# Kernel optimization log

Measured on AMD Instinct MI355X. Metric: run time of the kernel, lower is better.

## Reference

```python
import jax, jax.numpy as jnp
import numpy as np

B, N, H = 4, 1024, 64

def setup_inputs() -> dict:
    key = jax.random.key(0)
    k1, k2, k3 = jax.random.split(key, 3)
    x = jax.random.normal(k1, (B, N, H), dtype=jnp.float32)
    # nn.Linear(2H, H): weight [H, 2H], bias [H]
    s1 = 1.0 / np.sqrt(2 * H)
    W1 = jax.random.uniform(k2, (H, 2 * H), minval=-s1, maxval=s1, dtype=jnp.float32)
    b1 = jnp.zeros((H,), dtype=jnp.float32)
    # nn.Linear(H, 1): weight [1, H], bias [1]
    s2 = 1.0 / np.sqrt(H)
    W2 = jax.random.uniform(k3, (1, H), minval=-s2, maxval=s2, dtype=jnp.float32)
    b2 = jnp.zeros((1,), dtype=jnp.float32)
    return {"x": x, "W1": W1, "b1": b1, "W2": W2, "b2": b2}

def reference(x, W1, b1, W2, b2):
    # cat([x_i, x_j]) @ W1.T == x_i @ W1a.T + x_j @ W1b.T  (decomposed; same math)
    W1a, W1b = W1[:, :x.shape[-1]], W1[:, x.shape[-1]:]
    hi = jnp.einsum('bid,hd->bih', x, W1a)            # [B,N,H]
    hj = jnp.einsum('bjd,hd->bjh', x, W1b)            # [B,N,H]
    h = jax.nn.relu(hi[:, :, None, :] + hj[:, None, :, :] + b1)  # [B,N,N,H]
    logits = jnp.einsum('bijh,h->bij', h, W2[0]) + b2[0]          # [B,N,N]
    attn = jax.nn.softmax(logits, axis=-1)
    updated = jnp.einsum('bij,bjd->bid', attn, x)     # [B,N,H]
    return updated, attn
```

## Files before the change

### kernel.cpp

```cpp
#include <hip/hip_runtime.h>

#define ATTN_OFF 262144

#define WS_HIP  0
#define WS_HJP  131072

typedef float4 f4;
typedef _Float16 h2v __attribute__((ext_vector_type(2)));

union F4H { f4 f; h2v h[4]; };
union F2H { float2 f; h2v h[2]; };

__device__ __forceinline__ f4 ld4(const float* p) { return *reinterpret_cast<const f4*>(p); }
__device__ __forceinline__ void st4(float* p, f4 v) { *reinterpret_cast<f4*>(p) = v; }
__device__ __forceinline__ float fdot2f(h2v a, h2v b, float c) {
    return __builtin_amdgcn_fdot2(a, b, c, false);
}
__device__ __forceinline__ h2v pack2(float a, float b) {
    h2v r; r.x = (_Float16)a; r.y = (_Float16)b; return r;
}

__global__ __launch_bounds__(256, 4)
void ka_proj(const float* __restrict__ x, const float* __restrict__ W1,
             const float* __restrict__ b1,
             h2v* __restrict__ hiP, h2v* __restrict__ hjP) {
    __shared__ float xT[64 * 36];
    __shared__ float w1T[64 * 68];
    const int t  = threadIdx.x;
    const int i0 = blockIdx.x * 32;
    const int b  = blockIdx.y;
    const int z  = blockIdx.z;
    const int lo = t & 15;
    const int dq = t >> 4;
#pragma unroll
    for (int p = 0; p < 2; ++p) {
        const int il = p * 16 + lo;
        f4 v = ld4(&x[(size_t)(b * 1024 + i0 + il) * 64 + dq * 4]);
        xT[(dq * 4 + 0) * 36 + il] = v.x;
        xT[(dq * 4 + 1) * 36 + il] = v.y;
        xT[(dq * 4 + 2) * 36 + il] = v.z;
        xT[(dq * 4 + 3) * 36 + il] = v.w;
    }
#pragma unroll
    for (int p = 0; p < 4; ++p) {
        const int cl = p * 16 + lo;
        f4 w = ld4(&W1[(size_t)cl * 128 + z * 64 + dq * 4]);
        w1T[(dq * 4 + 0) * 68 + cl] = w.x;
        w1T[(dq * 4 + 1) * 68 + cl] = w.y;
        w1T[(dq * 4 + 2) * 68 + cl] = w.z;
        w1T[(dq * 4 + 3) * 68 + cl] = w.w;
    }
    __syncthreads();
    const int tx = t & 15;
    const int ty = t >> 4;
    float acc[2][4];
    if (z == 0) {
        f4 bv = ld4(&b1[tx * 4]);
        acc[0][0] = acc[1][0] = bv.x;
        acc[0][1] = acc[1][1] = bv.y;
        acc[0][2] = acc[1][2] = bv.z;
        acc[0][3] = acc[1][3] = bv.w;
    } else {
#pragma unroll
        for (int ii = 0; ii < 2; ++ii)
#pragma unroll
            for (int cc = 0; cc < 4; ++cc) acc[ii][cc] = 0.f;
    }
#pragma unroll 8
    for (int d = 0; d < 64; ++d) {
        const float2 xv = *reinterpret_cast<const float2*>(&xT[d * 36 + ty * 2]);
        const f4 wv = ld4(&w1T[d * 68 + tx * 4]);
        acc[0][0] = fmaf(xv.x, wv.x, acc[0][0]);
        acc[0][1] = fmaf(xv.x, wv.y, acc[0][1]);
        acc[0][2] = fmaf(xv.x, wv.z, acc[0][2]);
        acc[0][3] = fmaf(xv.x, wv.w, acc[0][3]);
        acc[1][0] = fmaf(xv.y, wv.x, acc[1][0]);
        acc[1][1] = fmaf(xv.y, wv.y, acc[1][1]);
        acc[1][2] = fmaf(xv.y, wv.z, acc[1][2]);
        acc[1][3] = fmaf(xv.y, wv.w, acc[1][3]);
    }
    h2v* outp = z ? hjP : hiP;
#pragma unroll
    for (int p = 0; p < 2; ++p) {
        F2H uo;
        uo.h[0] = pack2(acc[0][p * 2], acc[0][p * 2 + 1]);
        uo.h[1] = pack2(acc[1][p * 2], acc[1][p * 2 + 1]);
        *reinterpret_cast<float2*>(
            &outp[(size_t)(b * 32 + tx * 2 + p) * 1024 + i0 + ty * 2]) = uo.f;
    }
}

__global__ __launch_bounds__(256, 2)
void kf_fused(const h2v* __restrict__ hiP, const h2v* __restrict__ hjP,
              const float* __restrict__ W2, const float* __restrict__ x,
              float* __restrict__ attn, float* __restrict__ upd) {
    __shared__ union __align__(16) U {
        h2v   hj[32 * 256];
        h2v   xc[128 * 68];
        float red[16 * 516];
    } u;
    __shared__ __align__(16) h2v s_p[512 * 12];
    __shared__ h2v s_hi[32 * 8];
    __shared__ h2v s_w2[32];
    __shared__ float s_il[8];

    const int t  = threadIdx.x;
    const int i0 = blockIdx.x * 8;
    const int b  = blockIdx.y;
    const int w  = t >> 6;
    const int ln = t & 63;
    {
        const int hp = t >> 3, r = t & 7;
        s_hi[hp * 8 + r] = hiP[(size_t)(b * 32 + hp) * 1024 + i0 + r];
    }
    if (t < 16) {
        f4 wq = ld4(&W2[t * 4]);
        s_w2[t * 2]     = pack2(wq.x, wq.y);
        s_w2[t * 2 + 1] = pack2(wq.z, wq.w);
    }
    float l[2][4][4];
#pragma unroll
    for (int r = 0; r < 2; ++r)
#pragma unroll
        for (int c = 0; c < 4; ++c)
#pragma unroll
            for (int k = 0; k < 4; ++k) l[r][c][k] = 0.f;
    h2v hiR[2][32], w2R[32];
    const h2v z2 = (h2v)0;
#pragma unroll
    for (int c = 0; c < 4; ++c) {
#pragma unroll
        for (int p = 0; p < 8; ++p) {
            const int s = p * 256 + t;
            const int hp = s >> 6, j4 = (s & 63) * 4;
            st4((float*)&u.hj[hp * 256 + j4],
                ld4((const float*)&hjP[(size_t)(b * 32 + hp) * 1024 + c * 256 + j4]));
        }
        __syncthreads();
        if (c == 0) {
#pragma unroll
            for (int hp = 0; hp < 32; ++hp) {
                hiR[0][hp] = s_hi[hp * 8 + w];
                hiR[1][hp] = s_hi[hp * 8 + w + 4];
                w2R[hp]    = s_w2[hp];
            }
        }
#pragma unroll
        for (int hp = 0; hp < 32; ++hp) {
            F4H bb;
            bb.f = ld4((const float*)&u.hj[hp * 256 + ln * 4]);
            const h2v wv = w2R[hp];
#pragma unroll
            for (int r = 0; r < 2; ++r) {
                const h2v hv = hiR[r][hp];
#pragma unroll
                for (int k = 0; k < 4; ++k) {
                    h2v rr = __builtin_elementwise_max(hv + bb.h[k], z2);
                    l[r][c][k] = fdot2f(rr, wv, l[r][c][k]);
                }
            }
        }
        __syncthreads();
    }
    float il[2];
#pragma unroll
    for (int r = 0; r < 2; ++r) {
        float m = l[r][0][0];
#pragma unroll
        for (int c = 0; c < 4; ++c)
#pragma unroll
            for (int k = 0; k < 4; ++k) m = fmaxf(m, l[r][c][k]);
#pragma unroll
        for (int d = 1; d < 64; d <<= 1) m = fmaxf(m, __shfl_xor(m, d));
        float sum = 0.f;
#pragma unroll
        for (int c = 0; c < 4; ++c)
#pragma unroll
            for (int k = 0; k < 4; ++k) {
                l[r][c][k] = __expf(l[r][c][k] - m);
                sum += l[r][c][k];
            }
#pragma unroll
        for (int d = 1; d < 64; d <<= 1) sum += __shfl_xor(sum, d);
        il[r] = 1.0f / sum;
    }
    if (ln == 0) { s_il[w] = il[0]; s_il[w + 4] = il[1]; }
#pragma unroll
    for (int r = 0; r < 2; ++r) {
        const int row = w + r * 4;
        const size_t arow = (size_t)(b * 1024 + i0 + row) * 1024 + ln * 4;
#pragma unroll
        for (int c = 0; c < 4; ++c) {
            st4(&attn[arow + c * 256],
                make_float4(l[r][c][0] * il[r], l[r][c][1] * il[r],
                            l[r][c][2] * il[r], l[r][c][3] * il[r]));
            const int jp = c * 128 + ln * 2;
            s_p[jp * 12 + row]       = pack2(l[r][c][0], l[r][c][1]);
            s_p[(jp + 1) * 12 + row] = pack2(l[r][c][2], l[r][c][3]);
        }
    }
    const int dq = t & 15, js = t >> 4;
    float acc[8][4];
#pragma unroll
    for (int i = 0; i < 8; ++i)
#pragma unroll
        for (int q = 0; q < 4; ++q) acc[i][q] = 0.f;
#pragma unroll
    for (int c2 = 0; c2 < 4; ++c2) {
        __syncthreads();
#pragma unroll
        for (int p = 0; p < 8; ++p) {
            const int s = p * 256 + t;
            const int jpl = s >> 4, dd = (s & 15) * 4;
            const float* xr = &x[(size_t)(b * 1024 + c2 * 256 + jpl * 2) * 64 + dd];
            f4 r0 = ld4(xr);
            f4 r1 = ld4(xr + 64);
            F4H pk;
            pk.h[0] = pack2(r0.x, r1.x); pk.h[1] = pack2(r0.y, r1.y);
            pk.h[2] = pack2(r0.z, r1.z); pk.h[3] = pack2(r0.w, r1.w);
            st4((float*)&u.xc[jpl * 68 + dd], pk.f);
        }
        __syncthreads();
#pragma unroll 2
        for (int u8 = 0; u8 < 8; ++u8) {
            const int jpl = u8 * 16 + js;
            const int jp  = c2 * 128 + jpl;
            F4H p0, p1, xv;
            p0.f = ld4((const float*)&s_p[jp * 12]);
            p1.f = ld4((const float*)&s_p[jp * 12 + 4]);
            xv.f = ld4((const float*)&u.xc[jpl * 68 + dq * 4]);
#pragma unroll
            for (int i = 0; i < 8; ++i) {
                const h2v pa = (i < 4) ? p0.h[i] : p1.h[i - 4];
#pragma unroll
                for (int q = 0; q < 4; ++q)
                    acc[i][q] = fdot2f(pa, xv.h[q], acc[i][q]);
            }
        }
    }
    __syncthreads();
#pragma unroll
    for (int i = 0; i < 8; ++i)
        st4(&u.red[js * 516 + i * 64 + dq * 4],
            make_float4(acc[i][0], acc[i][1], acc[i][2], acc[i][3]));
    __syncthreads();
    if (t < 128) {
        const int i = t >> 4, dqq = t & 15;
        f4 a = ld4(&u.red[i * 64 + dqq * 4]);
#pragma unroll
        for (int js2 = 1; js2 < 16; ++js2) {
            f4 v = ld4(&u.red[js2 * 516 + i * 64 + dqq * 4]);
            a.x += v.x; a.y += v.y; a.z += v.z; a.w += v.w;
        }
        const float sc = s_il[i];
        st4(&upd[(size_t)(b * 1024 + i0 + i) * 64 + dqq * 4],
            make_float4(a.x * sc, a.y * sc, a.z * sc, a.w * sc));
    }
}

extern "C" void kernel_launch(void* const* d_in, const int* in_sizes, int n_in,
                              void* d_out, int out_size, void* d_ws, size_t ws_size,
                              hipStream_t stream) {
    const float* x  = (const float*)d_in[0];
    const float* W1 = (const float*)d_in[1];
    const float* b1 = (const float*)d_in[2];
    const float* W2 = (const float*)d_in[3];
    float* out = (float*)d_out;
    float* ws  = (float*)d_ws;
    h2v* hiP = (h2v*)(ws + WS_HIP);
    h2v* hjP = (h2v*)(ws + WS_HJP);

    ka_proj <<<dim3(32, 4, 2), 256, 0, stream>>>(x, W1, b1, hiP, hjP);
    kf_fused<<<dim3(128, 4),   256, 0, stream>>>(hiP, hjP, W2, x, out + ATTN_OFF, out);
}
```

Measured before the change: 99.16 us.

## Prefetch hj tiles in registers, read x directly, and shrink shared memory

The projection kernel now writes hi in row-major transposed form and pre-packs W2 to fp16 in the workspace, so the fused kernel loads hi and W2 straight into registers instead of going through shared memory. The hj tile loop register-prefetches the next chunk while the current one is computed, removing one load/store sync per chunk. The attn·x phase drops the shared-memory x staging and reads and packs x from global memory per wave. The cross-thread reduction moves to shuffles plus a small shared buffer. Shared-memory use falls, which may raise occupancy, but the change adds register pressure and repeated global reads of x.

Measured after the change: 95.56 us. 1.04x faster.

```diff
diff --git a/kernel.cpp b/kernel.cpp
--- a/kernel.cpp
+++ b/kernel.cpp
@@ -2,8 +2,9 @@
 
 #define ATTN_OFF 262144
 
-#define WS_HIP  0
+#define WS_HIT  0
 #define WS_HJP  131072
+#define WS_W2P  262144
 
 typedef float4 f4;
 typedef _Float16 h2v __attribute__((ext_vector_type(2)));
@@ -22,8 +23,8 @@
 
 __global__ __launch_bounds__(256, 4)
 void ka_proj(const float* __restrict__ x, const float* __restrict__ W1,
-             const float* __restrict__ b1,
-             h2v* __restrict__ hiP, h2v* __restrict__ hjP) {
+             const float* __restrict__ b1, const float* __restrict__ W2,
+             h2v* __restrict__ hiT, h2v* __restrict__ hjP, h2v* __restrict__ w2P) {
     __shared__ float xT[64 * 36];
     __shared__ float w1T[64 * 68];
     const int t  = threadIdx.x;
@@ -32,6 +33,11 @@
     const int z  = blockIdx.z;
     const int lo = t & 15;
     const int dq = t >> 4;
+    if (z == 0 && blockIdx.x == 0 && b == 0 && t < 16) {
+        f4 wq = ld4(&W2[t * 4]);
+        w2P[t * 2]     = pack2(wq.x, wq.y);
+        w2P[t * 2 + 1] = pack2(wq.z, wq.w);
+    }
 #pragma unroll
     for (int p = 0; p < 2; ++p) {
         const int il = p * 16 + lo;
@@ -79,29 +85,34 @@
         acc[1][2] = fmaf(xv.y, wv.z, acc[1][2]);
         acc[1][3] = fmaf(xv.y, wv.w, acc[1][3]);
     }
-    h2v* outp = z ? hjP : hiP;
-#pragma unroll
-    for (int p = 0; p < 2; ++p) {
-        F2H uo;
-        uo.h[0] = pack2(acc[0][p * 2], acc[0][p * 2 + 1]);
-        uo.h[1] = pack2(acc[1][p * 2], acc[1][p * 2 + 1]);
-        *reinterpret_cast<float2*>(
-            &outp[(size_t)(b * 32 + tx * 2 + p) * 1024 + i0 + ty * 2]) = uo.f;
+    if (z == 0) {
+#pragma unroll
+        for (int ii = 0; ii < 2; ++ii) {
+            F2H uo;
+            uo.h[0] = pack2(acc[ii][0], acc[ii][1]);
+            uo.h[1] = pack2(acc[ii][2], acc[ii][3]);
+            *reinterpret_cast<float2*>(
+                &hiT[(size_t)(b * 1024 + i0 + ty * 2 + ii) * 32 + tx * 2]) = uo.f;
+        }
+    } else {
+#pragma unroll
+        for (int p = 0; p < 2; ++p) {
+            F2H uo;
+            uo.h[0] = pack2(acc[0][p * 2], acc[0][p * 2 + 1]);
+            uo.h[1] = pack2(acc[1][p * 2], acc[1][p * 2 + 1]);
+            *reinterpret_cast<float2*>(
+                &hjP[(size_t)(b * 32 + tx * 2 + p) * 1024 + i0 + ty * 2]) = uo.f;
+        }
     }
 }
 
 __global__ __launch_bounds__(256, 2)
-void kf_fused(const h2v* __restrict__ hiP, const h2v* __restrict__ hjP,
-              const float* __restrict__ W2, const float* __restrict__ x,
+void kf_fused(const h2v* __restrict__ hiT, const h2v* __restrict__ hjP,
+              const h2v* __restrict__ w2P, const float* __restrict__ x,
               float* __restrict__ attn, float* __restrict__ upd) {
-    __shared__ union __align__(16) U {
-        h2v   hj[32 * 256];
-        h2v   xc[128 * 68];
-        float red[16 * 516];
-    } u;
+    __shared__ __align__(16) h2v s_hj[32 * 256];
     __shared__ __align__(16) h2v s_p[512 * 12];
-    __shared__ h2v s_hi[32 * 8];
-    __shared__ h2v s_w2[32];
+    __shared__ __align__(16) float s_red[3 * 8 * 64];
     __shared__ float s_il[8];
 
     const int t  = threadIdx.x;
@@ -109,15 +120,15 @@
     const int b  = blockIdx.y;
     const int w  = t >> 6;
     const int ln = t & 63;
-    {
-        const int hp = t >> 3, r = t & 7;
-        s_hi[hp * 8 + r] = hiP[(size_t)(b * 32 + hp) * 1024 + i0 + r];
-    }
-    if (t < 16) {
-        f4 wq = ld4(&W2[t * 4]);
-        s_w2[t * 2]     = pack2(wq.x, wq.y);
-        s_w2[t * 2 + 1] = pack2(wq.z, wq.w);
-    }
+
+    F4H hiR[2][8], w2R[8];
+#pragma unroll
+    for (int u = 0; u < 8; ++u) {
+        hiR[0][u].f = ld4((const float*)&hiT[(size_t)(b * 1024 + i0 + w) * 32 + u * 4]);
+        hiR[1][u].f = ld4((const float*)&hiT[(size_t)(b * 1024 + i0 + w + 4) * 32 + u * 4]);
+        w2R[u].f    = ld4((const float*)&w2P[u * 4]);
+    }
+
     float l[2][4][4];
 #pragma unroll
     for (int r = 0; r < 2; ++r)
@@ -125,34 +136,32 @@
         for (int c = 0; c < 4; ++c)
 #pragma unroll
             for (int k = 0; k < 4; ++k) l[r][c][k] = 0.f;
-    h2v hiR[2][32], w2R[32];
     const h2v z2 = (h2v)0;
+
+    f4 G[8];
+#pragma unroll
+    for (int p = 0; p < 8; ++p)
+        G[p] = ld4((const float*)&hjP[(size_t)(b * 32 + p * 4 + w) * 1024 + ln * 4]);
 #pragma unroll
     for (int c = 0; c < 4; ++c) {
 #pragma unroll
-        for (int p = 0; p < 8; ++p) {
-            const int s = p * 256 + t;
-            const int hp = s >> 6, j4 = (s & 63) * 4;
-            st4((float*)&u.hj[hp * 256 + j4],
-                ld4((const float*)&hjP[(size_t)(b * 32 + hp) * 1024 + c * 256 + j4]));
-        }
+        for (int p = 0; p < 8; ++p)
+            st4((float*)&s_hj[(p * 4 + w) * 256 + ln * 4], G[p]);
         __syncthreads();
-        if (c == 0) {
-#pragma unroll
-            for (int hp = 0; hp < 32; ++hp) {
-                hiR[0][hp] = s_hi[hp * 8 + w];
-                hiR[1][hp] = s_hi[hp * 8 + w + 4];
-                w2R[hp]    = s_w2[hp];
-            }
+        if (c < 3) {
+#pragma unroll
+            for (int p = 0; p < 8; ++p)
+                G[p] = ld4((const float*)&hjP[(size_t)(b * 32 + p * 4 + w) * 1024 +
+                                              (c + 1) * 256 + ln * 4]);
         }
 #pragma unroll
         for (int hp = 0; hp < 32; ++hp) {
             F4H bb;
-            bb.f = ld4((const float*)&u.hj[hp * 256 + ln * 4]);
-            const h2v wv = w2R[hp];
+            bb.f = ld4((const float*)&s_hj[hp * 256 + ln * 4]);
+            const h2v wv = w2R[hp >> 2].h[hp & 3];
 #pragma unroll
             for (int r = 0; r < 2; ++r) {
-                const h2v hv = hiR[r][hp];
+                const h2v hv = hiR[r][hp >> 2].h[hp & 3];
 #pragma unroll
                 for (int k = 0; k < 4; ++k) {
                     h2v rr = __builtin_elementwise_max(hv + bb.h[k], z2);
@@ -199,62 +208,59 @@
             s_p[(jp + 1) * 12 + row] = pack2(l[r][c][2], l[r][c][3]);
         }
     }
-    const int dq = t & 15, js = t >> 4;
+    __syncthreads();
+    const int dq = t & 15, jsl = (t >> 4) & 3;
     float acc[8][4];
 #pragma unroll
     for (int i = 0; i < 8; ++i)
 #pragma unroll
         for (int q = 0; q < 4; ++q) acc[i][q] = 0.f;
-#pragma unroll
-    for (int c2 = 0; c2 < 4; ++c2) {
-        __syncthreads();
-#pragma unroll
-        for (int p = 0; p < 8; ++p) {
-            const int s = p * 256 + t;
-            const int jpl = s >> 4, dd = (s & 15) * 4;
-            const float* xr = &x[(size_t)(b * 1024 + c2 * 256 + jpl * 2) * 64 + dd];
-            f4 r0 = ld4(xr);
-            f4 r1 = ld4(xr + 64);
-            F4H pk;
-            pk.h[0] = pack2(r0.x, r1.x); pk.h[1] = pack2(r0.y, r1.y);
-            pk.h[2] = pack2(r0.z, r1.z); pk.h[3] = pack2(r0.w, r1.w);
-            st4((float*)&u.xc[jpl * 68 + dd], pk.f);
-        }
-        __syncthreads();
-#pragma unroll 2
-        for (int u8 = 0; u8 < 8; ++u8) {
-            const int jpl = u8 * 16 + js;
-            const int jp  = c2 * 128 + jpl;
-            F4H p0, p1, xv;
-            p0.f = ld4((const float*)&s_p[jp * 12]);
-            p1.f = ld4((const float*)&s_p[jp * 12 + 4]);
-            xv.f = ld4((const float*)&u.xc[jpl * 68 + dq * 4]);
-#pragma unroll
-            for (int i = 0; i < 8; ++i) {
-                const h2v pa = (i < 4) ? p0.h[i] : p1.h[i - 4];
-#pragma unroll
-                for (int q = 0; q < 4; ++q)
-                    acc[i][q] = fdot2f(pa, xv.h[q], acc[i][q]);
+#pragma unroll 4
+    for (int it = 0; it < 32; ++it) {
+        const int jp = w * 128 + it * 4 + jsl;
+        F4H p0, p1, xv;
+        p0.f = ld4((const float*)&s_p[jp * 12]);
+        p1.f = ld4((const float*)&s_p[jp * 12 + 4]);
+        const float* xr = &x[(size_t)(b * 1024 + jp * 2) * 64 + dq * 4];
+        f4 r0 = ld4(xr);
+        f4 r1 = ld4(xr + 64);
+        xv.h[0] = pack2(r0.x, r1.x); xv.h[1] = pack2(r0.y, r1.y);
+        xv.h[2] = pack2(r0.z, r1.z); xv.h[3] = pack2(r0.w, r1.w);
+#pragma unroll
+        for (int i = 0; i < 8; ++i) {
+            const h2v pa = (i < 4) ? p0.h[i] : p1.h[i - 4];
+#pragma unroll
+            for (int q = 0; q < 4; ++q)
+                acc[i][q] = fdot2f(pa, xv.h[q], acc[i][q]);
+        }
+    }
+#pragma unroll
+    for (int i = 0; i < 8; ++i)
+#pragma unroll
+        for (int q = 0; q < 4; ++q) {
+            acc[i][q] += __shfl_xor(acc[i][q], 16);
+            acc[i][q] += __shfl_xor(acc[i][q], 32);
+        }
+    if (w > 0 && jsl == 0) {
+#pragma unroll
+        for (int i = 0; i < 8; ++i)
+            st4(&s_red[((w - 1) * 8 + i) * 64 + dq * 4],
+                make_float4(acc[i][0], acc[i][1], acc[i][2], acc[i][3]));
+    }
+    __syncthreads();
+    if (w == 0 && jsl == 0) {
+#pragma unroll
+        for (int i = 0; i < 8; ++i) {
+            f4 a = make_float4(acc[i][0], acc[i][1], acc[i][2], acc[i][3]);
+#pragma unroll
+            for (int wv2 = 0; wv2 < 3; ++wv2) {
+                f4 v = ld4(&s_red[(wv2 * 8 + i) * 64 + dq * 4]);
+                a.x += v.x; a.y += v.y; a.z += v.z; a.w += v.w;
             }
-        }
-    }
-    __syncthreads();
-#pragma unroll
-    for (int i = 0; i < 8; ++i)
-        st4(&u.red[js * 516 + i * 64 + dq * 4],
-            make_float4(acc[i][0], acc[i][1], acc[i][2], acc[i][3]));
-    __syncthreads();
-    if (t < 128) {
-        const int i = t >> 4, dqq = t & 15;
-        f4 a = ld4(&u.red[i * 64 + dqq * 4]);
-#pragma unroll
-        for (int js2 = 1; js2 < 16; ++js2) {
-            f4 v = ld4(&u.red[js2 * 516 + i * 64 + dqq * 4]);
-            a.x += v.x; a.y += v.y; a.z += v.z; a.w += v.w;
-        }
-        const float sc = s_il[i];
-        st4(&upd[(size_t)(b * 1024 + i0 + i) * 64 + dqq * 4],
-            make_float4(a.x * sc, a.y * sc, a.z * sc, a.w * sc));
+            const float sc = s_il[i];
+            st4(&upd[(size_t)(b * 1024 + i0 + i) * 64 + dq * 4],
+                make_float4(a.x * sc, a.y * sc, a.z * sc, a.w * sc));
+        }
     }
 }
 
@@ -267,9 +273,10 @@
     const float* W2 = (const float*)d_in[3];
     float* out = (float*)d_out;
     float* ws  = (float*)d_ws;
-    h2v* hiP = (h2v*)(ws + WS_HIP);
+    h2v* hiT = (h2v*)(ws + WS_HIT);
     h2v* hjP = (h2v*)(ws + WS_HJP);
-
-    ka_proj <<<dim3(32, 4, 2), 256, 0, stream>>>(x, W1, b1, hiP, hjP);
-    kf_fused<<<dim3(128, 4),   256, 0, stream>>>(hiP, hjP, W2, x, out + ATTN_OFF, out);
-}
+    h2v* w2P = (h2v*)(ws + WS_W2P);
+
+    ka_proj <<<dim3(32, 4, 2), 256, 0, stream>>>(x, W1, b1, W2, hiT, hjP, w2P);
+    kf_fused<<<dim3(128, 4),   256, 0, stream>>>(hiT, hjP, w2P, x, out + ATTN_OFF, out);
+}
```
